# Optimization experiments

Hardware: AMD Instinct MI355X
Metric: run time of the kernel (lower is better)

## Reference

```python
import jax, jax.numpy as jnp
import numpy as np

TOPK = 2
NUM_EXPERTS = 8

def setup_inputs() -> dict:
    key = jax.random.key(0)
    kx, kg, k1, k3, k2 = jax.random.split(key, 5)
    B, S, D, F, E = 1, 2048, 1024, 1024, NUM_EXPERTS
    x = jax.random.normal(kx, (B, S, D), dtype=jnp.float32)
    wg = jax.random.normal(kg, (E, D), dtype=jnp.float32) * (1.0 / np.sqrt(D))
    w1 = jax.random.normal(k1, (E, D, F), dtype=jnp.float32) * (1.0 / np.sqrt(D))
    w3 = jax.random.normal(k3, (E, D, F), dtype=jnp.float32) * (1.0 / np.sqrt(D))
    w2 = jax.random.normal(k2, (E, F, D), dtype=jnp.float32) * (1.0 / np.sqrt(F))
    return {"x": x, "wg": wg, "w1": w1, "w3": w3, "w2": w2}

def reference(x, wg, w1, w3, w2):
    # x: [B, S, D] -> tokens [N, D]
    D = x.shape[-1]
    E = wg.shape[0]
    xt = x.reshape(-1, D)
    # Gating: Linear(no bias) + softmax over experts
    logits = xt @ wg.T                      # [N, E]
    gates = jax.nn.softmax(logits, axis=-1)
    # Top-k selection, normalize weights (normalize_expert_weights=True),
    # routed_scaling_factor = 1.0
    weights, idx = jax.lax.top_k(gates, TOPK)      # [N, k]
    weights = weights / weights.sum(axis=-1, keepdims=True)
    # Per-token per-expert combine weight (dispatch+combine equivalent)
    comb = (jax.nn.one_hot(idx, E, dtype=xt.dtype) * weights[..., None]).sum(axis=1)  # [N, E]
    # SwiGLU experts (grouped GEMM equivalent, dense over experts)
    h = jnp.einsum('nd,edf->enf', xt, w1)   # gate proj
    u = jnp.einsum('nd,edf->enf', xt, w3)   # up proj
    a = jax.nn.silu(h) * u                  # [E, N, F]
    out = jnp.einsum('enf,efd,ne->nd', a, w2, comb)
    return out.reshape(x.shape), logits
```

## Files before the change

kernel.cpp:

```cpp
#include <hip/hip_runtime.h>
#include <stdint.h>

typedef unsigned short u16;
typedef __attribute__((ext_vector_type(8))) __bf16 bf16x8;
typedef __attribute__((ext_vector_type(4))) float f32x4;

#define MAXMT 40
#define N_TOK 2048
#define DDIM 1024
#define FDIM 1024

#define DEV static __device__ __forceinline__

DEV float bf2f(u16 u) {
    union { uint32_t i; float f; } v;
    v.i = ((uint32_t)u) << 16;
    return v.f;
}
DEV u16 f2bf(float f) {
    union { float f; uint32_t i; } v;
    v.f = f;
    uint32_t x = v.i;
    return (u16)((x + 0x7fffu + ((x >> 16) & 1u)) >> 16);
}

DEV void async_copy16(const u16* gsrc, u16* ldst) {
    __builtin_amdgcn_global_load_lds(
        (const __attribute__((address_space(1))) void*)(uintptr_t)gsrc,
        (__attribute__((address_space(3))) void*)(uint32_t)(uintptr_t)ldst,
        16, 0, 0);
}

DEV int sniff_fp(const void* p, int tid, int* scnt) {
    if (tid == 0) *scnt = 0;
    __syncthreads();
    u16 u = ((const u16*)p)[tid & 255];
    int e = (u >> 7) & 0xff;
    if (e != 0 && (e < 90 || e > 160)) atomicAdd(scnt, 1);
    __syncthreads();
    return *scnt > 64;
}

__global__ void k_mega(const void* __restrict__ x, const void* __restrict__ wg,
                       const void* __restrict__ w1, const void* __restrict__ w3,
                       const void* __restrict__ w2, u16* __restrict__ wt,
                       u16* __restrict__ xb, void* __restrict__ out_base,
                       int* __restrict__ te, float* __restrict__ tw) {
    __shared__ int scnt;
    __shared__ __align__(16) u16 s2[64 * 68];
    int z = blockIdx.z, tid = threadIdx.x;

    if (z < 24) {
        int which = z >> 3, mat = z & 7;
        const void* src0 = which == 0 ? w1 : (which == 1 ? w3 : w2);
        int fp = sniff_fp(src0, tid, &scnt);
        u16* dst = wt + ((size_t)z) * 1048576;
        int rg = tid >> 4, cg = tid & 15;
        int r0 = blockIdx.y * 64, c0 = blockIdx.x * 64;
        int rbase = r0 + rg * 4, cbase = c0 + cg * 4;

        u16 v[4][4];
        if (fp) {
            const float* sp = (const float*)src0 + (size_t)mat * 1048576;
#pragma unroll
            for (int i = 0; i < 4; i++) {
                float4 f = *(const float4*)(sp + (size_t)(rbase + i) * 1024 + cbase);
                v[i][0] = f2bf(f.x); v[i][1] = f2bf(f.y);
                v[i][2] = f2bf(f.z); v[i][3] = f2bf(f.w);
            }
        } else {
            const u16* sp = (const u16*)src0 + (size_t)mat * 1048576;
#pragma unroll
            for (int i = 0; i < 4; i++)
                *(uint2*)&v[i][0] = *(const uint2*)(sp + (size_t)(rbase + i) * 1024 + cbase);
        }
#pragma unroll
        for (int j = 0; j < 4; j++) {
            uint32_t lo = (uint32_t)v[0][j] | ((uint32_t)v[1][j] << 16);
            uint32_t hi = (uint32_t)v[2][j] | ((uint32_t)v[3][j] << 16);
            uint2 w; w.x = lo; w.y = hi;
            *(uint2*)&s2[(cg * 4 + j) * 68 + rg * 4] = w;
        }
        __syncthreads();
        int cc = tid >> 2, seg = tid & 3;
        const u16* spp = &s2[cc * 68 + seg * 16];
        uint2 q0 = *(const uint2*)(spp);
        uint2 q1 = *(const uint2*)(spp + 4);
        uint2 q2 = *(const uint2*)(spp + 8);
        uint2 q3 = *(const uint2*)(spp + 12);
        u16* dp = dst + (size_t)(c0 + cc) * 1024 + r0 + seg * 16;
        uint4 o0, o1;
        o0.x = q0.x; o0.y = q0.y; o0.z = q1.x; o0.w = q1.y;
        o1.x = q2.x; o1.y = q2.y; o1.z = q3.x; o1.w = q3.y;
        *(uint4*)dp = o0;
        *(uint4*)(dp + 8) = o1;
    } else {
        int fp = sniff_fp(x, tid, &scnt);
        int gi = (z - 24) * 256 + blockIdx.y * 16 + blockIdx.x;
        int wave = tid >> 6, lane = tid & 63;
        int n = gi * 4 + wave;
        float acc[8];
#pragma unroll
        for (int e = 0; e < 8; e++) acc[e] = 0.f;
        if (fp) {
            const float* xp = (const float*)x + (size_t)n * DDIM;
            const float* wp = (const float*)wg;
            for (int it = 0; it < 16; ++it) {
                int d = it * 64 + lane;
                float xv = xp[d];
                xb[(size_t)n * DDIM + d] = f2bf(xv);
#pragma unroll
                for (int e = 0; e < 8; e++) acc[e] += xv * wp[e * DDIM + d];
            }
        } else {
            const u16* xp = (const u16*)x + (size_t)n * DDIM;
            const u16* wp = (const u16*)wg;
            for (int it = 0; it < 16; ++it) {
                int d = it * 64 + lane;
                u16 raw = xp[d];
                xb[(size_t)n * DDIM + d] = raw;
                float xv = bf2f(raw);
#pragma unroll
                for (int e = 0; e < 8; e++) acc[e] += xv * bf2f(wp[e * DDIM + d]);
            }
        }
#pragma unroll
        for (int e = 0; e < 8; e++) {
            for (int off = 32; off; off >>= 1) acc[e] += __shfl_xor(acc[e], off);
        }
        if (lane < 8) {
            if (fp) ((float*)out_base + (size_t)N_TOK * DDIM)[n * 8 + lane] = acc[lane];
            else    ((u16*)out_base + (size_t)N_TOK * DDIM)[n * 8 + lane] = f2bf(acc[lane]);
        }
        if (lane == 0) {
            int e0 = 0; float b0 = acc[0];
            for (int e = 1; e < 8; e++) if (acc[e] > b0) { b0 = acc[e]; e0 = e; }
            int e1 = -1; float b1 = -1e30f;
            for (int e = 0; e < 8; e++) if (e != e0 && acc[e] > b1) { b1 = acc[e]; e1 = e; }
            float m = fmaxf(b0, b1);
            float x0 = __expf(b0 - m), x1 = __expf(b1 - m);
            float sden = x0 + x1;
            te[n * 2] = e0; te[n * 2 + 1] = e1;
            tw[n * 2] = x0 / sden; tw[n * 2 + 1] = x1 / sden;
        }
    }
}

__global__ void k_sched(const int* __restrict__ te, const float* __restrict__ tw,
                        int* __restrict__ pair_token, float* __restrict__ pair_weight,
                        int* __restrict__ ppos, int* __restrict__ sched) {
    __shared__ int cnt[8], cur[8];
    int t = threadIdx.x;
    if (t < 8) cnt[t] = 0;
    __syncthreads();
    for (int n = t; n < N_TOK; n += 256) {
        atomicAdd(&cnt[te[2 * n]], 1);
        atomicAdd(&cnt[te[2 * n + 1]], 1);
    }
    __syncthreads();
    if (t == 0) {
        int o = 0, mt = 0;
        for (int e = 0; e < 8; e++) {
            cur[e] = o;
            int c = cnt[e];
            for (int m0 = 0; m0 < c; m0 += 128) {
                sched[mt] = e;
                sched[MAXMT + mt] = o + m0;
                sched[2 * MAXMT + mt] = (c - m0 < 128) ? (c - m0) : 128;
                mt++;
            }
            o += c;
        }
        sched[3 * MAXMT] = mt;
        for (int i = mt; i < MAXMT; i++) { sched[i] = 0; sched[MAXMT + i] = 0; sched[2 * MAXMT + i] = 0; }
    }
    __syncthreads();
    for (int n = t; n < N_TOK; n += 256) {
#pragma unroll
        for (int s = 0; s < 2; s++) {
            int e = te[2 * n + s];
            int p = atomicAdd(&cur[e], 1);
            pair_token[p] = n;
            pair_weight[p] = tw[2 * n + s];
            ppos[2 * n + s] = p;
        }
    }
}

__launch_bounds__(256, 3)
__global__ void k_gemm13(const u16* __restrict__ xb, const u16* __restrict__ w1t,
                         const u16* __restrict__ w3t, const int* __restrict__ pair_token,
                         const int* __restrict__ sched, u16* __restrict__ Abuf) {
    __shared__ __align__(16) u16 smem[16384];
    u16* sA  = smem;
    u16* sB1 = smem + 8192;
    u16* sB3 = smem + 12288;

    int bn = blockIdx.x;
    int bm = blockIdx.y;
    int total = sched[3 * MAXMT];
    if (bm >= total) return;
    int e = sched[bm];
    int row0 = sched[MAXMT + bm];
    int rowsv = sched[2 * MAXMT + bm];

    int tid = threadIdx.x;
    int wave = tid >> 6, lane = tid & 63;
    int wm = wave & 1, wn = wave >> 1;
    int quad = lane >> 4, l15 = lane & 15;
    int lsub = lane >> 3, slot = lane & 7;

    const u16* gA[4]; u16* lA[4];
#pragma unroll
    for (int c = 0; c < 4; c++) {
        int row = c * 32 + wave * 8 + lsub;
        int cr = row < rowsv ? row : 0;
        int tok = pair_token[row0 + cr];
        int gch = slot ^ (row & 7);
        gA[c] = xb + (size_t)tok * DDIM + gch * 8;
        lA[c] = sA + c * 2048 + wave * 512;
    }
    const u16* gB1[2]; const u16* gB3[2]; int lBoff[2];
#pragma unroll
    for (int c = 0; c < 2; c++) {
        int row = c * 32 + wave * 8 + lsub;
        int gch = slot ^ (row & 7);
        int fcol = bn * 64 + row;
        gB1[c] = w1t + ((size_t)e * 1024 + fcol) * 1024 + gch * 8;
        gB3[c] = w3t + ((size_t)e * 1024 + fcol) * 1024 + gch * 8;
        lBoff[c] = c * 2048 + wave * 512;
    }

    f32x4 acc_h[4][2], acc_u[4][2];
#pragma unroll
    for (int i = 0; i < 4; i++)
#pragma unroll
        for (int j = 0; j < 2; j++) { acc_h[i][j] = (f32x4)0.f; acc_u[i][j] = (f32x4)0.f; }

    for (int kt = 0; kt < 16; ++kt) {
        int k0 = kt * 64;
        __syncthreads();
#pragma unroll
        for (int c = 0; c < 4; c++) async_copy16(gA[c] + k0, lA[c]);
#pragma unroll
        for (int c = 0; c < 2; c++) {
            async_copy16(gB1[c] + k0, sB1 + lBoff[c]);
            async_copy16(gB3[c] + k0, sB3 + lBoff[c]);
        }
        __syncthreads();
#pragma unroll
        for (int kk = 0; kk < 2; ++kk) {
            bf16x8 a[4], b1[2], b3[2];
#pragma unroll
            for (int i = 0; i < 4; i++) {
                int m = wm * 64 + i * 16 + l15;
                int s = (kk * 4 + quad) ^ (m & 7);
                a[i] = *(const bf16x8*)&sA[m * 64 + s * 8];
            }
#pragma unroll
            for (int j = 0; j < 2; j++) {
                int nn = wn * 32 + j * 16 + l15;
                int s = (kk * 4 + quad) ^ (nn & 7);
                b1[j] = *(const bf16x8*)&sB1[nn * 64 + s * 8];
                b3[j] = *(const bf16x8*)&sB3[nn * 64 + s * 8];
            }
#pragma unroll
            for (int i = 0; i < 4; i++)
#pragma unroll
                for (int j = 0; j < 2; j++) {
                    acc_h[i][j] = __builtin_amdgcn_mfma_f32_16x16x32_bf16(a[i], b1[j], acc_h[i][j], 0, 0, 0);
                    acc_u[i][j] = __builtin_amdgcn_mfma_f32_16x16x32_bf16(a[i], b3[j], acc_u[i][j], 0, 0, 0);
                }
        }
    }
    __syncthreads();
#pragma unroll
    for (int i = 0; i < 4; i++)
#pragma unroll
        for (int j = 0; j < 2; j++)
#pragma unroll
            for (int r = 0; r < 4; r++) {
                int row = wm * 64 + i * 16 + quad * 4 + r;
                int col = wn * 32 + j * 16 + l15;
                float h = acc_h[i][j][r], u = acc_u[i][j][r];
                smem[row * 72 + col] = f2bf(h * u / (1.0f + __expf(-h)));
            }
    __syncthreads();
    int rt = tid >> 1, half = tid & 1;
    if (rt < rowsv) {
        u16* dp = Abuf + (size_t)(row0 + rt) * FDIM + bn * 64 + half * 32;
        const u16* sp = &smem[rt * 72 + half * 32];
#pragma unroll
        for (int q = 0; q < 4; q++)
            *(uint4*)(dp + q * 8) = *(const uint4*)(sp + q * 8);
    }
}

__launch_bounds__(256, 3)
__global__ void k_gemm2(const u16* __restrict__ Abuf, const u16* __restrict__ w2t,
                        const int* __restrict__ sched, u16* __restrict__ Ybuf) {
    __shared__ __align__(16) u16 smem[12288];
    u16* sA = smem;
    u16* sB = smem + 8192;

    int bn = blockIdx.x;
    int bm = blockIdx.y;
    int total = sched[3 * MAXMT];
    if (bm >= total) return;
    int e = sched[bm];
    int row0 = sched[MAXMT + bm];
    int rowsv = sched[2 * MAXMT + bm];

    int tid = threadIdx.x;
    int wave = tid >> 6, lane = tid & 63;
    int wm = wave & 1, wn = wave >> 1;
    int quad = lane >> 4, l15 = lane & 15;
    int lsub = lane >> 3, slot = lane & 7;

    const u16* gA[4]; u16* lA[4];
#pragma unroll
    for (int c = 0; c < 4; c++) {
        int row = c * 32 + wave * 8 + lsub;
        int cr = row < rowsv ? row : 0;
        int gch = slot ^ (row & 7);
        gA[c] = Abuf + (size_t)(row0 + cr) * FDIM + gch * 8;
        lA[c] = sA + c * 2048 + wave * 512;
    }
    const u16* gB[2]; u16* lB[2];
#pragma unroll
    for (int c = 0; c < 2; c++) {
        int row = c * 32 + wave * 8 + lsub;
        int gch = slot ^ (row & 7);
        int dcol = bn * 64 + row;
        gB[c] = w2t + ((size_t)e * 1024 + dcol) * 1024 + gch * 8;
        lB[c] = sB + c * 2048 + wave * 512;
    }

    f32x4 acc[4][2];
#pragma unroll
    for (int i = 0; i < 4; i++)
#pragma unroll
        for (int j = 0; j < 2; j++) acc[i][j] = (f32x4)0.f;

    for (int kt = 0; kt < 16; ++kt) {
        int k0 = kt * 64;
        __syncthreads();
#pragma unroll
        for (int c = 0; c < 4; c++) async_copy16(gA[c] + k0, lA[c]);
#pragma unroll
        for (int c = 0; c < 2; c++) async_copy16(gB[c] + k0, lB[c]);
        __syncthreads();
#pragma unroll
        for (int kk = 0; kk < 2; ++kk) {
            bf16x8 a[4], b[2];
#pragma unroll
            for (int i = 0; i < 4; i++) {
                int m = wm * 64 + i * 16 + l15;
                int s = (kk * 4 + quad) ^ (m & 7);
                a[i] = *(const bf16x8*)&sA[m * 64 + s * 8];
            }
#pragma unroll
            for (int j = 0; j < 2; j++) {
                int nn = wn * 32 + j * 16 + l15;
                int s = (kk * 4 + quad) ^ (nn & 7);
                b[j] = *(const bf16x8*)&sB[nn * 64 + s * 8];
            }
#pragma unroll
            for (int i = 0; i < 4; i++)
#pragma unroll
                for (int j = 0; j < 2; j++)
                    acc[i][j] = __builtin_amdgcn_mfma_f32_16x16x32_bf16(a[i], b[j], acc[i][j], 0, 0, 0);
        }
    }
    __syncthreads();
#pragma unroll
    for (int i = 0; i < 4; i++)
#pragma unroll
        for (int j = 0; j < 2; j++)
#pragma unroll
            for (int r = 0; r < 4; r++) {
                int row = wm * 64 + i * 16 + quad * 4 + r;
                int col = wn * 32 + j * 16 + l15;
                smem[row * 72 + col] = f2bf(acc[i][j][r]);
            }
    __syncthreads();
    int rt = tid >> 1, half = tid & 1;
    if (rt < rowsv) {
        u16* dp = Ybuf + (size_t)(row0 + rt) * DDIM + bn * 64 + half * 32;
        const u16* sp = &smem[rt * 72 + half * 32];
#pragma unroll
        for (int q = 0; q < 4; q++)
            *(uint4*)(dp + q * 8) = *(const uint4*)(sp + q * 8);
    }
}

__global__ void k_combine(const u16* __restrict__ Y, const int* __restrict__ ppos,
                          const float* __restrict__ pwt, const void* __restrict__ x,
                          void* __restrict__ out) {
    __shared__ int scnt;
    int n = blockIdx.x, t = threadIdx.x;
    int fp = sniff_fp(x, t, &scnt);
    int p0 = ppos[2 * n], p1 = ppos[2 * n + 1];
    float w0 = pwt[p0], w1 = pwt[p1];
    uint2 a = *(const uint2*)(Y + (size_t)p0 * 1024 + t * 4);
    uint2 b = *(const uint2*)(Y + (size_t)p1 * 1024 + t * 4);
    const u16* ap = (const u16*)&a;
    const u16* bp = (const u16*)&b;
    float r[4];
#pragma unroll
    for (int j = 0; j < 4; j++) r[j] = w0 * bf2f(ap[j]) + w1 * bf2f(bp[j]);
    if (fp) {
        float4 o = { r[0], r[1], r[2], r[3] };
        *(float4*)((float*)out + (size_t)n * 1024 + t * 4) = o;
    } else {
        u16 o[4] = { f2bf(r[0]), f2bf(r[1]), f2bf(r[2]), f2bf(r[3]) };
        *(uint2*)((u16*)out + (size_t)n * 1024 + t * 4) = *(const uint2*)o;
    }
}

extern "C" void kernel_launch(void* const* d_in, const int* in_sizes, int n_in,
                              void* d_out, int out_size, void* d_ws, size_t ws_size,
                              hipStream_t stream) {
    const void* x  = d_in[0];
    const void* wg = d_in[1];
    const void* w1 = d_in[2];
    const void* w3 = d_in[3];
    const void* w2 = d_in[4];

    u16* wt   = (u16*)d_ws;
    u16* w1t  = wt;
    u16* w3t  = wt + (size_t)8 * 1048576;
    u16* w2t  = wt + (size_t)16 * 1048576;
    u16* Abuf = wt + (size_t)24 * 1048576;
    u16* Ybuf = Abuf + (size_t)4096 * 1024;
    u16* xb   = Ybuf + (size_t)4096 * 1024;
    int*   te   = (int*)(xb + (size_t)N_TOK * DDIM);
    float* tw   = (float*)(te + 2 * N_TOK);
    int*   ptok = (int*)(tw + 2 * N_TOK);
    float* pwt  = (float*)(ptok + 2 * N_TOK);
    int*   ppos = (int*)(pwt + 2 * N_TOK);
    int*   sched = ppos + 2 * N_TOK;

    k_mega<<<dim3(16, 16, 26), 256, 0, stream>>>(x, wg, w1, w3, w2, wt, xb, d_out, te, tw);
    k_sched<<<1, 256, 0, stream>>>(te, tw, ptok, pwt, ppos, sched);
    k_gemm13<<<dim3(16, MAXMT), 256, 0, stream>>>(xb, w1t, w3t, ptok, sched, Abuf);
    k_gemm2<<<dim3(16, MAXMT), 256, 0, stream>>>(Abuf, w2t, sched, Ybuf);
    k_combine<<<2048, 256, 0, stream>>>(Ybuf, ppos, pwt, x, d_out);
}
```

Measured before the change: 203.9 us.

## Double-buffer LDS tiles in expert GEMMs and vectorize gating loads

Both expert GEMM kernels now use two LDS buffers. The next K-tile's async copies are issued before computing on the current tile, leaving one barrier per iteration instead of two, so global loads can overlap MFMA work. The gating pass now reads x and wg with 4-wide vector loads, and the prep kernel puts the gating blocks at the lowest z indices so they are scheduled first. The cost is twice the LDS per block, which lowers k_gemm13's launch bound to 2 blocks per CU and may reduce occupancy.

```diff
diff --git a/kernel.cpp b/kernel.cpp
--- a/kernel.cpp
+++ b/kernel.cpp
@@ -50,11 +50,12 @@
     __shared__ __align__(16) u16 s2[64 * 68];
     int z = blockIdx.z, tid = threadIdx.x;
 
-    if (z < 24) {
-        int which = z >> 3, mat = z & 7;
+    if (z >= 2) {
+        int zz = z - 2;
+        int which = zz >> 3, mat = zz & 7;
         const void* src0 = which == 0 ? w1 : (which == 1 ? w3 : w2);
         int fp = sniff_fp(src0, tid, &scnt);
-        u16* dst = wt + ((size_t)z) * 1048576;
+        u16* dst = wt + ((size_t)zz) * 1048576;
         int rg = tid >> 4, cg = tid & 15;
         int r0 = blockIdx.y * 64, c0 = blockIdx.x * 64;
         int rbase = r0 + rg * 4, cbase = c0 + cg * 4;
@@ -96,7 +97,7 @@
         *(uint4*)(dp + 8) = o1;
     } else {
         int fp = sniff_fp(x, tid, &scnt);
-        int gi = (z - 24) * 256 + blockIdx.y * 16 + blockIdx.x;
+        int gi = z * 256 + blockIdx.y * 16 + blockIdx.x;
         int wave = tid >> 6, lane = tid & 63;
         int n = gi * 4 + wave;
         float acc[8];
@@ -105,23 +106,34 @@
         if (fp) {
             const float* xp = (const float*)x + (size_t)n * DDIM;
             const float* wp = (const float*)wg;
-            for (int it = 0; it < 16; ++it) {
-                int d = it * 64 + lane;
-                float xv = xp[d];
-                xb[(size_t)n * DDIM + d] = f2bf(xv);
-#pragma unroll
-                for (int e = 0; e < 8; e++) acc[e] += xv * wp[e * DDIM + d];
+#pragma unroll
+            for (int it = 0; it < 4; ++it) {
+                int d = it * 256 + lane * 4;
+                float4 xv = *(const float4*)(xp + d);
+                u16 pk[4] = { f2bf(xv.x), f2bf(xv.y), f2bf(xv.z), f2bf(xv.w) };
+                *(uint2*)&xb[(size_t)n * DDIM + d] = *(const uint2*)pk;
+#pragma unroll
+                for (int e = 0; e < 8; e++) {
+                    float4 w4 = *(const float4*)(wp + e * DDIM + d);
+                    acc[e] += xv.x * w4.x + xv.y * w4.y + xv.z * w4.z + xv.w * w4.w;
+                }
             }
         } else {
             const u16* xp = (const u16*)x + (size_t)n * DDIM;
             const u16* wp = (const u16*)wg;
-            for (int it = 0; it < 16; ++it) {
-                int d = it * 64 + lane;
-                u16 raw = xp[d];
-                xb[(size_t)n * DDIM + d] = raw;
-                float xv = bf2f(raw);
-#pragma unroll
-                for (int e = 0; e < 8; e++) acc[e] += xv * bf2f(wp[e * DDIM + d]);
+#pragma unroll
+            for (int it = 0; it < 4; ++it) {
+                int d = it * 256 + lane * 4;
+                uint2 raw = *(const uint2*)(xp + d);
+                *(uint2*)&xb[(size_t)n * DDIM + d] = raw;
+                const u16* rp = (const u16*)&raw;
+                float x0 = bf2f(rp[0]), x1 = bf2f(rp[1]), x2 = bf2f(rp[2]), x3 = bf2f(rp[3]);
+#pragma unroll
+                for (int e = 0; e < 8; e++) {
+                    uint2 wr = *(const uint2*)(wp + e * DDIM + d);
+                    const u16* wq = (const u16*)&wr;
+                    acc[e] += x0 * bf2f(wq[0]) + x1 * bf2f(wq[1]) + x2 * bf2f(wq[2]) + x3 * bf2f(wq[3]);
+                }
             }
         }
 #pragma unroll
@@ -187,14 +199,11 @@
     }
 }
 
-__launch_bounds__(256, 3)
+__launch_bounds__(256, 2)
 __global__ void k_gemm13(const u16* __restrict__ xb, const u16* __restrict__ w1t,
                          const u16* __restrict__ w3t, const int* __restrict__ pair_token,
                          const int* __restrict__ sched, u16* __restrict__ Abuf) {
-    __shared__ __align__(16) u16 smem[16384];
-    u16* sA  = smem;
-    u16* sB1 = smem + 8192;
-    u16* sB3 = smem + 12288;
+    __shared__ __align__(16) u16 smem[32768];
 
     int bn = blockIdx.x;
     int bm = blockIdx.y;
@@ -210,7 +219,7 @@
     int quad = lane >> 4, l15 = lane & 15;
     int lsub = lane >> 3, slot = lane & 7;
 
-    const u16* gA[4]; u16* lA[4];
+    const u16* gA[4]; int aoff[4];
 #pragma unroll
     for (int c = 0; c < 4; c++) {
         int row = c * 32 + wave * 8 + lsub;
@@ -218,9 +227,9 @@
         int tok = pair_token[row0 + cr];
         int gch = slot ^ (row & 7);
         gA[c] = xb + (size_t)tok * DDIM + gch * 8;
-        lA[c] = sA + c * 2048 + wave * 512;
-    }
-    const u16* gB1[2]; const u16* gB3[2]; int lBoff[2];
+        aoff[c] = c * 2048 + wave * 512;
+    }
+    const u16* gB1[2]; const u16* gB3[2]; int b1off[2], b3off[2];
 #pragma unroll
     for (int c = 0; c < 2; c++) {
         int row = c * 32 + wave * 8 + lsub;
@@ -228,7 +237,8 @@
         int fcol = bn * 64 + row;
         gB1[c] = w1t + ((size_t)e * 1024 + fcol) * 1024 + gch * 8;
         gB3[c] = w3t + ((size_t)e * 1024 + fcol) * 1024 + gch * 8;
-        lBoff[c] = c * 2048 + wave * 512;
+        b1off[c] = 8192 + c * 2048 + wave * 512;
+        b3off[c] = 12288 + c * 2048 + wave * 512;
     }
 
     f32x4 acc_h[4][2], acc_u[4][2];
@@ -237,17 +247,32 @@
 #pragma unroll
         for (int j = 0; j < 2; j++) { acc_h[i][j] = (f32x4)0.f; acc_u[i][j] = (f32x4)0.f; }
 
+#pragma unroll
+    for (int c = 0; c < 4; c++) async_copy16(gA[c], smem + aoff[c]);
+#pragma unroll
+    for (int c = 0; c < 2; c++) {
+        async_copy16(gB1[c], smem + b1off[c]);
+        async_copy16(gB3[c], smem + b3off[c]);
+    }
+
     for (int kt = 0; kt < 16; ++kt) {
-        int k0 = kt * 64;
+        int cur = kt & 1;
+        u16* sbuf = smem + cur * 16384;
         __syncthreads();
-#pragma unroll
-        for (int c = 0; c < 4; c++) async_copy16(gA[c] + k0, lA[c]);
-#pragma unroll
-        for (int c = 0; c < 2; c++) {
-            async_copy16(gB1[c] + k0, sB1 + lBoff[c]);
-            async_copy16(gB3[c] + k0, sB3 + lBoff[c]);
-        }
-        __syncthreads();
+        if (kt < 15) {
+            int k1 = (kt + 1) * 64;
+            u16* nbuf = smem + (cur ^ 1) * 16384;
+#pragma unroll
+            for (int c = 0; c < 4; c++) async_copy16(gA[c] + k1, nbuf + aoff[c]);
+#pragma unroll
+            for (int c = 0; c < 2; c++) {
+                async_copy16(gB1[c] + k1, nbuf + b1off[c]);
+                async_copy16(gB3[c] + k1, nbuf + b3off[c]);
+            }
+        }
+        const u16* sA_  = sbuf;
+        const u16* sB1_ = sbuf + 8192;
+        const u16* sB3_ = sbuf + 12288;
 #pragma unroll
         for (int kk = 0; kk < 2; ++kk) {
             bf16x8 a[4], b1[2], b3[2];
@@ -255,14 +280,14 @@
             for (int i = 0; i < 4; i++) {
                 int m = wm * 64 + i * 16 + l15;
                 int s = (kk * 4 + quad) ^ (m & 7);
-                a[i] = *(const bf16x8*)&sA[m * 64 + s * 8];
+                a[i] = *(const bf16x8*)&sA_[m * 64 + s * 8];
             }
 #pragma unroll
             for (int j = 0; j < 2; j++) {
                 int nn = wn * 32 + j * 16 + l15;
                 int s = (kk * 4 + quad) ^ (nn & 7);
-                b1[j] = *(const bf16x8*)&sB1[nn * 64 + s * 8];
-                b3[j] = *(const bf16x8*)&sB3[nn * 64 + s * 8];
+                b1[j] = *(const bf16x8*)&sB1_[nn * 64 + s * 8];
+                b3[j] = *(const bf16x8*)&sB3_[nn * 64 + s * 8];
             }
 #pragma unroll
             for (int i = 0; i < 4; i++)
@@ -299,9 +324,7 @@
 __launch_bounds__(256, 3)
 __global__ void k_gemm2(const u16* __restrict__ Abuf, const u16* __restrict__ w2t,
                         const int* __restrict__ sched, u16* __restrict__ Ybuf) {
-    __shared__ __align__(16) u16 smem[12288];
-    u16* sA = smem;
-    u16* sB = smem + 8192;
+    __shared__ __align__(16) u16 smem[24576];
 
     int bn = blockIdx.x;
     int bm = blockIdx.y;
@@ -317,23 +340,23 @@
     int quad = lane >> 4, l15 = lane & 15;
     int lsub = lane >> 3, slot = lane & 7;
 
-    const u16* gA[4]; u16* lA[4];
+    const u16* gA[4]; int aoff[4];
 #pragma unroll
     for (int c = 0; c < 4; c++) {
         int row = c * 32 + wave * 8 + lsub;
         int cr = row < rowsv ? row : 0;
         int gch = slot ^ (row & 7);
         gA[c] = Abuf + (size_t)(row0 + cr) * FDIM + gch * 8;
-        lA[c] = sA + c * 2048 + wave * 512;
-    }
-    const u16* gB[2]; u16* lB[2];
+        aoff[c] = c * 2048 + wave * 512;
+    }
+    const u16* gB[2]; int boff[2];
 #pragma unroll
     for (int c = 0; c < 2; c++) {
         int row = c * 32 + wave * 8 + lsub;
         int gch = slot ^ (row & 7);
         int dcol = bn * 64 + row;
         gB[c] = w2t + ((size_t)e * 1024 + dcol) * 1024 + gch * 8;
-        lB[c] = sB + c * 2048 + wave * 512;
+        boff[c] = 8192 + c * 2048 + wave * 512;
     }
 
     f32x4 acc[4][2];
@@ -342,14 +365,25 @@
 #pragma unroll
         for (int j = 0; j < 2; j++) acc[i][j] = (f32x4)0.f;
 
+#pragma unroll
+    for (int c = 0; c < 4; c++) async_copy16(gA[c], smem + aoff[c]);
+#pragma unroll
+    for (int c = 0; c < 2; c++) async_copy16(gB[c], smem + boff[c]);
+
     for (int kt = 0; kt < 16; ++kt) {
-        int k0 = kt * 64;
+        int cur = kt & 1;
+        u16* sbuf = smem + cur * 12288;
         __syncthreads();
-#pragma unroll
-        for (int c = 0; c < 4; c++) async_copy16(gA[c] + k0, lA[c]);
-#pragma unroll
-        for (int c = 0; c < 2; c++) async_copy16(gB[c] + k0, lB[c]);
-        __syncthreads();
+        if (kt < 15) {
+            int k1 = (kt + 1) * 64;
+            u16* nbuf = smem + (cur ^ 1) * 12288;
+#pragma unroll
+            for (int c = 0; c < 4; c++) async_copy16(gA[c] + k1, nbuf + aoff[c]);
+#pragma unroll
+            for (int c = 0; c < 2; c++) async_copy16(gB[c] + k1, nbuf + boff[c]);
+        }
+        const u16* sA_ = sbuf;
+        const u16* sB_ = sbuf + 8192;
 #pragma unroll
         for (int kk = 0; kk < 2; ++kk) {
             bf16x8 a[4], b[2];
@@ -357,13 +391,13 @@
             for (int i = 0; i < 4; i++) {
                 int m = wm * 64 + i * 16 + l15;
                 int s = (kk * 4 + quad) ^ (m & 7);
-                a[i] = *(const bf16x8*)&sA[m * 64 + s * 8];
+                a[i] = *(const bf16x8*)&sA_[m * 64 + s * 8];
             }
 #pragma unroll
             for (int j = 0; j < 2; j++) {
                 int nn = wn * 32 + j * 16 + l15;
                 int s = (kk * 4 + quad) ^ (nn & 7);
-                b[j] = *(const bf16x8*)&sB[nn * 64 + s * 8];
+                b[j] = *(const bf16x8*)&sB_[nn * 64 + s * 8];
             }
 #pragma unroll
             for (int i = 0; i < 4; i++)
```

Result: no change. 203.9 us (-0.0%).
